# Optimization experiments

Hardware: AMD Instinct MI355X
Metric: run time of the kernel (lower is better)

The kernel has to match this reference:

```python
import jax, jax.numpy as jnp
import numpy as np

N_NODES = 100000
N_EDGES = 3200000
N_GRAPHS = 64


def setup_inputs() -> dict:
    key = jax.random.key(0)
    ks = jax.random.split(key, 9)
    x = jax.random.normal(ks[0], (N_NODES, 3), dtype=jnp.float32)
    edge_index = jax.random.randint(ks[1], (2, N_EDGES), 0, N_NODES, dtype=jnp.int64)
    batch = jnp.sort(jax.random.randint(ks[2], (N_NODES,), 0, N_GRAPHS, dtype=jnp.int64))
    s1 = 1.0 / np.sqrt(3.0)
    s2 = 1.0 / np.sqrt(64.0)
    W1 = jax.random.normal(ks[3], (3, 64), dtype=jnp.float32) * s1
    b1 = jax.random.normal(ks[4], (64,), dtype=jnp.float32) * 0.02
    W2 = jax.random.normal(ks[5], (64, 64), dtype=jnp.float32) * s2
    b2 = jax.random.normal(ks[6], (64,), dtype=jnp.float32) * 0.02
    Wr = jax.random.normal(ks[7], (64, 1), dtype=jnp.float32) * s2
    br = jax.random.normal(ks[8], (1,), dtype=jnp.float32) * 0.02
    return {"x": x, "edge_index": edge_index, "batch": batch,
            "W1": W1, "b1": b1, "W2": W2, "b2": b2, "Wr": Wr, "br": br}


def reference(x, edge_index, batch, W1, b1, W2, b2, Wr, br):
    N = x.shape[0]
    # GCN normalization with self-loops: A_hat = D^-1/2 (A+I) D^-1/2
    loop = jnp.arange(N, dtype=edge_index.dtype)
    src = jnp.concatenate([edge_index[0], loop])  # message sources
    dst = jnp.concatenate([edge_index[1], loop])  # aggregation targets
    deg = jax.ops.segment_sum(jnp.ones(src.shape, jnp.float32), dst, num_segments=N)
    dinv = jnp.where(deg > 0, jax.lax.rsqrt(deg), 0.0)
    norm = dinv[src] * dinv[dst]  # [E+N]

    def conv(h):  # h: [N, F] -> gather, scale, scatter-add
        return jax.ops.segment_sum(norm[:, None] * h[src], dst, num_segments=N)

    h = jax.nn.relu(conv(x @ W1) + b1)
    # dropout(p=0.5) is identity in eval mode
    h = jax.nn.relu(conv(h @ W2) + b2)
    # global mean pool over graphs
    counts = jax.ops.segment_sum(jnp.ones((N,), jnp.float32), batch, num_segments=N_GRAPHS)
    pooled = jax.ops.segment_sum(h, batch, num_segments=N_GRAPHS) / jnp.maximum(counts, 1.0)[:, None]
    return pooled @ Wr + br
```

## Files before the change

kernel.cpp:

```cpp
#include <hip/hip_runtime.h>

#define N_NODES  100000
#define N_EDGES  3200000
#define N_GRAPHS 64
#define NBUCK 391
#define BSH   8
#define TILE  4096
#define CSR_CAP 9216

typedef float v2f __attribute__((ext_vector_type(2)));

__device__ __forceinline__ unsigned pk8(float a, float b, float c, float d) {
    int r = 0;
    r = __builtin_amdgcn_cvt_pk_fp8_f32(a, b, r, false);
    r = __builtin_amdgcn_cvt_pk_fp8_f32(c, d, r, true);
    return (unsigned)r;
}
__device__ __forceinline__ void addfp8(float4& a, unsigned u) {
    v2f lo = __builtin_amdgcn_cvt_pk_f32_fp8((int)u, false);
    v2f hi = __builtin_amdgcn_cvt_pk_f32_fp8((int)u, true);
    a.x += lo[0]; a.y += lo[1]; a.z += hi[0]; a.w += hi[1];
}
__device__ __forceinline__ void fma4(float4& c, float s, const float4& w) {
    c.x += s * w.x; c.y += s * w.y; c.z += s * w.z; c.w += s * w.w;
}

__global__ __launch_bounds__(1024) void k_split(
        const int* __restrict__ src, const int* __restrict__ dst,
        int* __restrict__ gcur, unsigned int* __restrict__ ebuf, int E) {
    __shared__ int hist[512];
    __shared__ int excl_s[512];
    __shared__ int base[NBUCK];
    __shared__ int curs[NBUCK];
    __shared__ int wtot[8];
    __shared__ unsigned int stg[TILE];
    __shared__ unsigned short bkt[TILE];
    int t = threadIdx.x;
    if (t < 512) hist[t] = 0;
    __syncthreads();

    int e0 = blockIdx.x * TILE;
    int nvalid = min(TILE, E - e0);
    int es[4], ed[4];
#pragma unroll
    for (int k = 0; k < 4; ++k) {
        int i = e0 + t + k * 1024;
        if (i < E) {
            es[k] = src[i]; ed[k] = dst[i];
            atomicAdd(&hist[ed[k] >> BSH], 1);
        } else { es[k] = 0; ed[k] = -1; }
    }
    __syncthreads();
    int v = (t < 512) ? hist[t] : 0;
    int lane = t & 63, wvi = t >> 6;
    int val = v;
    for (int off = 1; off < 64; off <<= 1) {
        int u = __shfl_up(val, off);
        if (lane >= off) val += u;
    }
    if (t < 512 && lane == 63) wtot[wvi] = val;
    __syncthreads();
    if (t < 512) {
        int woff = 0;
        for (int w = 0; w < wvi; ++w) woff += wtot[w];
        int texcl = woff + val - v;
        excl_s[t] = texcl;
        if (t < NBUCK) {
            if (v > 0) base[t] = atomicAdd(&gcur[t], v);
            curs[t] = 0;
        }
    }
    __syncthreads();
#pragma unroll
    for (int k = 0; k < 4; ++k) {
        if (ed[k] >= 0) {
            int b = ed[k] >> BSH;
            int r = atomicAdd(&curs[b], 1);
            int pos = excl_s[b] + r;
            stg[pos] = ((unsigned)(ed[k] & 255) << 24) | (unsigned)es[k];
            bkt[pos] = (unsigned short)b;
        }
    }
    __syncthreads();
    for (int j = t; j < nvalid; j += 1024) {
        unsigned p = stg[j];
        int b = bkt[j];
        int pos = base[b] + (j - excl_s[b]);
        if (pos < CSR_CAP) ebuf[(size_t)b * CSR_CAP + pos] = p;
    }
}

__global__ __launch_bounds__(1024) void k_csr(
        const unsigned int* __restrict__ ebuf, const int* __restrict__ gcur,
        int* __restrict__ rowptr, float* __restrict__ dinv, float4* __restrict__ y4,
        const float* __restrict__ x, int* __restrict__ csr_src, int N) {
    __shared__ int ncnt[256];
    __shared__ int nbase[256];
    __shared__ int ncur[256];
    __shared__ int wtot[4];
    __shared__ int sbase;
    __shared__ int stg[CSR_CAP];
    int b = blockIdx.x, t = threadIdx.x;
    int node0 = b << BSH;
    int nodes = min(256, N - node0);
    int cntE = min(gcur[b], CSR_CAP);
    const unsigned int* eb = ebuf + (size_t)b * CSR_CAP;
    if (t < 64) {
        int acc = 0;
        for (int i = t; i < b; i += 64) acc += min(gcur[i], CSR_CAP);
        for (int off = 32; off > 0; off >>= 1) acc += __shfl_down(acc, off);
        if (t == 0) sbase = acc;
    }
    if (t < 256) { ncnt[t] = 0; ncur[t] = 0; }
    __syncthreads();
    int base = sbase;
    if (b == NBUCK - 1 && t == 0) rowptr[N_NODES] = base + cntE;
    for (int j = t; j < cntE; j += 1024) atomicAdd(&ncnt[(int)(eb[j] >> 24)], 1);
    __syncthreads();
    int v = (t < 256) ? ncnt[t] : 0;
    if (t < 256) {
        int lane = t & 63, wv = t >> 6;
        int val = v;
        for (int off = 1; off < 64; off <<= 1) {
            int u = __shfl_up(val, off);
            if (lane >= off) val += u;
        }
        if (lane == 63) wtot[wv] = val;
        __syncthreads();
        int woff = 0;
        for (int w = 0; w < wv; ++w) woff += wtot[w];
        int excl = woff + val - v;
        nbase[t] = excl;
        if (t < nodes) {
            int nn = node0 + t;
            rowptr[nn] = base + excl;
            float dn = rsqrtf((float)(v + 1));
            dinv[nn] = dn;
            y4[nn] = make_float4(dn * x[nn * 3 + 0], dn * x[nn * 3 + 1], dn * x[nn * 3 + 2], 0.f);
        }
    } else {
        __syncthreads();
    }
    __syncthreads();
    for (int j = t; j < cntE; j += 1024) {
        unsigned p = eb[j];
        int ln = (int)(p >> 24);
        int r = atomicAdd(&ncur[ln], 1);
        stg[nbase[ln] + r] = (int)(p & 0xFFFFFFu);
    }
    __syncthreads();
    for (int j = t; j < cntE; j += 1024) csr_src[(size_t)base + j] = stg[j];
}

__global__ __launch_bounds__(256) void k_agg3h1(
        const float4* __restrict__ y4, const int* __restrict__ csr_src,
        const int* __restrict__ rowptr, const float* __restrict__ dinv,
        const float* __restrict__ W1, const float* __restrict__ b1,
        uint4* __restrict__ Hs, int N) {
    int tid = blockIdx.x * blockDim.x + threadIdx.x;
    int n = tid >> 2, q = tid & 3;
    if (n >= N) return;
    int beg = rowptr[n], end = rowptr[n + 1];
    float ax0 = 0.f, ay0 = 0.f, az0 = 0.f;
    float ax1 = 0.f, ay1 = 0.f, az1 = 0.f;
    float ax2 = 0.f, ay2 = 0.f, az2 = 0.f;
    float ax3 = 0.f, ay3 = 0.f, az3 = 0.f;
    if (end > beg) {
        for (int c = beg; c < end; c += 32) {
            int idx[8];
#pragma unroll
            for (int j = 0; j < 8; ++j)
                idx[j] = csr_src[min(c + 4 * j + q, end - 1)];
            float4 v[8];
#pragma unroll
            for (int j = 0; j < 8; ++j) v[j] = y4[idx[j]];
#pragma unroll
            for (int j = 0; j < 8; ++j) {
                bool ok = (c + 4 * j + q) < end;
                float vx = ok ? v[j].x : 0.f;
                float vy = ok ? v[j].y : 0.f;
                float vz = ok ? v[j].z : 0.f;
                if ((j & 3) == 0) { ax0 += vx; ay0 += vy; az0 += vz; }
                if ((j & 3) == 1) { ax1 += vx; ay1 += vy; az1 += vz; }
                if ((j & 3) == 2) { ax2 += vx; ay2 += vy; az2 += vz; }
                if ((j & 3) == 3) { ax3 += vx; ay3 += vy; az3 += vz; }
            }
        }
    }
    float rx = (ax0 + ax1) + (ax2 + ax3);
    float ry = (ay0 + ay1) + (ay2 + ay3);
    float rz = (az0 + az1) + (az2 + az3);
    for (int off = 1; off < 4; off <<= 1) {
        rx += __shfl_xor(rx, off);
        ry += __shfl_xor(ry, off);
        rz += __shfl_xor(rz, off);
    }
    float dn = dinv[n];
    float4 self = y4[n];
    float A0 = dn * (rx + self.x), A1 = dn * (ry + self.y), A2 = dn * (rz + self.z);
    unsigned vals[4];
#pragma unroll
    for (int g = 0; g < 4; ++g) {
        int f = 16 * q + 4 * g;
        float w0 = dn * fmaxf(A0 * W1[f]     + A1 * W1[64 + f]     + A2 * W1[128 + f]     + b1[f],     0.f);
        float w1 = dn * fmaxf(A0 * W1[f + 1] + A1 * W1[64 + f + 1] + A2 * W1[128 + f + 1] + b1[f + 1], 0.f);
        float w2 = dn * fmaxf(A0 * W1[f + 2] + A1 * W1[64 + f + 2] + A2 * W1[128 + f + 2] + b1[f + 2], 0.f);
        float w3 = dn * fmaxf(A0 * W1[f + 3] + A1 * W1[64 + f + 3] + A2 * W1[128 + f + 3] + b1[f + 3], 0.f);
        vals[g] = pk8(w0, w1, w2, w3);
    }
    Hs[(size_t)n * 4 + q] = make_uint4(vals[0], vals[1], vals[2], vals[3]);
}

__global__ __launch_bounds__(256) void k_agg(
        const unsigned int* __restrict__ Hs, const int* __restrict__ csr_src,
        const int* __restrict__ rowptr, const float* __restrict__ dinv,
        float* __restrict__ out, int N) {
    int tid = blockIdx.x * blockDim.x + threadIdx.x;
    int n = tid >> 4, q = tid & 15;
    if (n >= N) return;
    int lane = threadIdx.x & 63;
    int base = lane & ~15;
    int beg = rowptr[n], end = rowptr[n + 1];
    float4 acc0 = make_float4(0.f, 0.f, 0.f, 0.f);
    float4 acc1 = make_float4(0.f, 0.f, 0.f, 0.f);
    float4 acc2 = make_float4(0.f, 0.f, 0.f, 0.f);
    float4 acc3 = make_float4(0.f, 0.f, 0.f, 0.f);
    if (end > beg) {
        int myidx = csr_src[min(beg + q, end - 1)];
        for (int c = beg; c < end; c += 16) {
            int nxt = csr_src[min(c + 16 + q, end - 1)];
            unsigned u[16];
#pragma unroll
            for (int j = 0; j < 16; ++j) {
                int s = __shfl(myidx, base + j);
                u[j] = Hs[(size_t)s * 16 + q];
            }
            int m = end - c;
#pragma unroll
            for (int j = 0; j < 16; ++j) {
                unsigned uj = (j < m) ? u[j] : 0u;
                if ((j & 3) == 0) addfp8(acc0, uj);
                if ((j & 3) == 1) addfp8(acc1, uj);
                if ((j & 3) == 2) addfp8(acc2, uj);
                if ((j & 3) == 3) addfp8(acc3, uj);
            }
            myidx = nxt;
        }
    }
    addfp8(acc0, Hs[(size_t)n * 16 + q]);
    float dn = dinv[n];
    float4 r;
    r.x = dn * ((acc0.x + acc1.x) + (acc2.x + acc3.x));
    r.y = dn * ((acc0.y + acc1.y) + (acc2.y + acc3.y));
    r.z = dn * ((acc0.z + acc1.z) + (acc2.z + acc3.z));
    r.w = dn * ((acc0.w + acc1.w) + (acc2.w + acc3.w));
    ((float4*)(out + (size_t)n * 64))[q] = r;
}

__global__ __launch_bounds__(256) void k_mmpool(
        const float4* __restrict__ A4, const float4* __restrict__ W2v,
        const float* __restrict__ b2, const float* __restrict__ Wr,
        const int* __restrict__ batch, float* __restrict__ gsum,
        float* __restrict__ gcnt, int N) {
    __shared__ float4 W2s[1024];
    __shared__ float lsum[N_GRAPHS];
    __shared__ float lcnt[N_GRAPHS];
    int t = threadIdx.x;
    for (int i = t; i < 1024; i += 256) W2s[i] = W2v[i];
    if (t < N_GRAPHS) { lsum[t] = 0.f; lcnt[t] = 0.f; }
    __syncthreads();

    int f4 = t & 15;
    int ng = t >> 4;
    float4 bb = ((const float4*)b2)[f4];
    float4 wr = ((const float4*)Wr)[f4];
    int base = blockIdx.x * 128;

    for (int tile = 0; tile < 2; ++tile) {
        int n0 = base + tile * 64 + ng * 4;
        int m0 = min(n0 + 0, N - 1), m1 = min(n0 + 1, N - 1);
        int m2 = min(n0 + 2, N - 1), m3 = min(n0 + 3, N - 1);
        const float4* r0 = A4 + (size_t)m0 * 16;
        const float4* r1 = A4 + (size_t)m1 * 16;
        const float4* r2 = A4 + (size_t)m2 * 16;
        const float4* r3 = A4 + (size_t)m3 * 16;
        float4 c0 = make_float4(0.f, 0.f, 0.f, 0.f);
        float4 c1 = make_float4(0.f, 0.f, 0.f, 0.f);
        float4 c2 = make_float4(0.f, 0.f, 0.f, 0.f);
        float4 c3 = make_float4(0.f, 0.f, 0.f, 0.f);
#pragma unroll 4
        for (int ks = 0; ks < 16; ++ks) {
            float4 a0 = r0[ks], a1 = r1[ks], a2 = r2[ks], a3 = r3[ks];
            float4 w0 = W2s[(4 * ks + 0) * 16 + f4];
            float4 w1 = W2s[(4 * ks + 1) * 16 + f4];
            float4 w2 = W2s[(4 * ks + 2) * 16 + f4];
            float4 w3 = W2s[(4 * ks + 3) * 16 + f4];
            fma4(c0, a0.x, w0); fma4(c0, a0.y, w1); fma4(c0, a0.z, w2); fma4(c0, a0.w, w3);
            fma4(c1, a1.x, w0); fma4(c1, a1.y, w1); fma4(c1, a1.z, w2); fma4(c1, a1.w, w3);
            fma4(c2, a2.x, w0); fma4(c2, a2.y, w1); fma4(c2, a2.z, w2); fma4(c2, a2.w, w3);
            fma4(c3, a3.x, w0); fma4(c3, a3.y, w1); fma4(c3, a3.z, w2); fma4(c3, a3.w, w3);
        }
        float p0 = fmaxf(c0.x + bb.x, 0.f) * wr.x + fmaxf(c0.y + bb.y, 0.f) * wr.y +
                   fmaxf(c0.z + bb.z, 0.f) * wr.z + fmaxf(c0.w + bb.w, 0.f) * wr.w;
        float p1 = fmaxf(c1.x + bb.x, 0.f) * wr.x + fmaxf(c1.y + bb.y, 0.f) * wr.y +
                   fmaxf(c1.z + bb.z, 0.f) * wr.z + fmaxf(c1.w + bb.w, 0.f) * wr.w;
        float p2 = fmaxf(c2.x + bb.x, 0.f) * wr.x + fmaxf(c2.y + bb.y, 0.f) * wr.y +
                   fmaxf(c2.z + bb.z, 0.f) * wr.z + fmaxf(c2.w + bb.w, 0.f) * wr.w;
        float p3 = fmaxf(c3.x + bb.x, 0.f) * wr.x + fmaxf(c3.y + bb.y, 0.f) * wr.y +
                   fmaxf(c3.z + bb.z, 0.f) * wr.z + fmaxf(c3.w + bb.w, 0.f) * wr.w;
        for (int off = 8; off > 0; off >>= 1) {
            p0 += __shfl_down(p0, off);
            p1 += __shfl_down(p1, off);
            p2 += __shfl_down(p2, off);
            p3 += __shfl_down(p3, off);
        }
        if (f4 == 0) {
            if (n0 + 0 < N) { int g = batch[n0 + 0]; atomicAdd(&lsum[g], p0); atomicAdd(&lcnt[g], 1.f); }
            if (n0 + 1 < N) { int g = batch[n0 + 1]; atomicAdd(&lsum[g], p1); atomicAdd(&lcnt[g], 1.f); }
            if (n0 + 2 < N) { int g = batch[n0 + 2]; atomicAdd(&lsum[g], p2); atomicAdd(&lcnt[g], 1.f); }
            if (n0 + 3 < N) { int g = batch[n0 + 3]; atomicAdd(&lsum[g], p3); atomicAdd(&lcnt[g], 1.f); }
        }
    }
    __syncthreads();
    if (t < N_GRAPHS && lcnt[t] > 0.0f) {
        atomicAdd(&gsum[t], lsum[t]);
        atomicAdd(&gcnt[t], lcnt[t]);
    }
}

__global__ void k_out(const float* __restrict__ gsum, const float* __restrict__ gcnt,
                      const float* __restrict__ br, float* __restrict__ out) {
    int g = threadIdx.x;
    if (g < N_GRAPHS) out[g] = gsum[g] / fmaxf(gcnt[g], 1.0f) + br[0];
}

extern "C" void kernel_launch(void* const* d_in, const int* in_sizes, int n_in,
                              void* d_out, int out_size, void* d_ws, size_t ws_size,
                              hipStream_t stream) {
    const float* x     = (const float*)d_in[0];
    const int*   ei    = (const int*)d_in[1];
    const int*   batch = (const int*)d_in[2];
    const float* W1    = (const float*)d_in[3];
    const float* b1    = (const float*)d_in[4];
    const float* W2    = (const float*)d_in[5];
    const float* b2    = (const float*)d_in[6];
    const float* Wr    = (const float*)d_in[7];
    const float* br    = (const float*)d_in[8];
    float* out = (float*)d_out;

    const int N = N_NODES, E = N_EDGES;
    const int* src = ei;
    const int* dst = ei + E;

    char* w = (char*)d_ws;
    float* A        = (float*)w; w += (size_t)N * 64 * sizeof(float);
    unsigned int* Hs = (unsigned int*)w; w += (size_t)N * 64;
    int*   csr_src  = (int*)w;   w += (size_t)E * sizeof(int);
    float* dinv     = (float*)w; w += (size_t)N * sizeof(float);
    int*   rowptr   = (int*)w;   w += (size_t)(N + 1) * sizeof(int);
    int*   gcur     = (int*)w;   w += (size_t)NBUCK * sizeof(int);
    float* gsum     = (float*)w; w += N_GRAPHS * sizeof(float);
    float* gcnt     = (float*)w; w += N_GRAPHS * sizeof(float);
    float4* y4      = (float4*)w; w += (size_t)N * sizeof(float4);
    unsigned int* ebuf = (unsigned int*)A;

    hipMemsetAsync(gcur, 0, (size_t)NBUCK * sizeof(int), stream);
    hipMemsetAsync(gsum, 0, N_GRAPHS * sizeof(float), stream);
    hipMemsetAsync(gcnt, 0, N_GRAPHS * sizeof(float), stream);

    k_split<<<(E + TILE - 1) / TILE, 1024, 0, stream>>>(src, dst, gcur, ebuf, E);
    k_csr<<<NBUCK, 1024, 0, stream>>>(ebuf, gcur, rowptr, dinv, y4, x, csr_src, N);

    k_agg3h1<<<(N * 4 + 255) / 256, 256, 0, stream>>>(y4, csr_src, rowptr, dinv,
                                                      W1, b1, (uint4*)Hs, N);

    k_agg<<<(N * 16 + 255) / 256, 256, 0, stream>>>(Hs, csr_src, rowptr, dinv, A, N);
    k_mmpool<<<(N + 127) / 128, 256, 0, stream>>>((const float4*)A, (const float4*)W2,
                                                  b2, Wr, batch, gsum, gcnt, N);

    k_out<<<1, 64, 0, stream>>>(gsum, gcnt, br, out);
}
```

Baseline: 214.0 us.

## Use 16-byte gathers in layer-2 aggregation with cross-lane feature reduction

Each 16-lane node group now splits into 4 edge-parallel subgroups of 4 lanes. Each lane loads a uint4 (16 fp8 features) per neighbor instead of one 4-byte word, so the gather uses fewer, wider memory transactions. Partial sums are combined across subgroups with xor shuffles, and the per-edge broadcast shuffle of source indices is removed. Index loads are nontemporal and prefetched only when another chunk exists. The cost is extra shuffle reduction work and a changed output write pattern.

```diff
diff --git a/kernel.cpp b/kernel.cpp
--- a/kernel.cpp
+++ b/kernel.cpp
@@ -212,49 +212,63 @@
 }
 
 __global__ __launch_bounds__(256) void k_agg(
-        const unsigned int* __restrict__ Hs, const int* __restrict__ csr_src,
+        const uint4* __restrict__ Hs4, const int* __restrict__ csr_src,
         const int* __restrict__ rowptr, const float* __restrict__ dinv,
         float* __restrict__ out, int N) {
     int tid = blockIdx.x * blockDim.x + threadIdx.x;
-    int n = tid >> 4, q = tid & 15;
+    int n = tid >> 4, sub = tid & 15;
     if (n >= N) return;
-    int lane = threadIdx.x & 63;
-    int base = lane & ~15;
+    int p = sub >> 2;
+    int f = sub & 3;
     int beg = rowptr[n], end = rowptr[n + 1];
-    float4 acc0 = make_float4(0.f, 0.f, 0.f, 0.f);
-    float4 acc1 = make_float4(0.f, 0.f, 0.f, 0.f);
-    float4 acc2 = make_float4(0.f, 0.f, 0.f, 0.f);
-    float4 acc3 = make_float4(0.f, 0.f, 0.f, 0.f);
+    float4 a0 = make_float4(0.f, 0.f, 0.f, 0.f);
+    float4 a1 = make_float4(0.f, 0.f, 0.f, 0.f);
+    float4 a2 = make_float4(0.f, 0.f, 0.f, 0.f);
+    float4 a3 = make_float4(0.f, 0.f, 0.f, 0.f);
     if (end > beg) {
-        int myidx = csr_src[min(beg + q, end - 1)];
+        int e[4];
+#pragma unroll
+        for (int j = 0; j < 4; ++j)
+            e[j] = __builtin_nontemporal_load(&csr_src[min(beg + 4 * j + p, end - 1)]);
         for (int c = beg; c < end; c += 16) {
-            int nxt = csr_src[min(c + 16 + q, end - 1)];
-            unsigned u[16];
-#pragma unroll
-            for (int j = 0; j < 16; ++j) {
-                int s = __shfl(myidx, base + j);
-                u[j] = Hs[(size_t)s * 16 + q];
+            uint4 u[4];
+#pragma unroll
+            for (int j = 0; j < 4; ++j)
+                u[j] = Hs4[(size_t)e[j] * 4 + f];
+            int c2 = c + 16;
+            if (c2 < end) {
+#pragma unroll
+                for (int j = 0; j < 4; ++j)
+                    e[j] = __builtin_nontemporal_load(&csr_src[min(c2 + 4 * j + p, end - 1)]);
             }
             int m = end - c;
 #pragma unroll
-            for (int j = 0; j < 16; ++j) {
-                unsigned uj = (j < m) ? u[j] : 0u;
-                if ((j & 3) == 0) addfp8(acc0, uj);
-                if ((j & 3) == 1) addfp8(acc1, uj);
-                if ((j & 3) == 2) addfp8(acc2, uj);
-                if ((j & 3) == 3) addfp8(acc3, uj);
+            for (int j = 0; j < 4; ++j) {
+                uint4 uu = u[j];
+                if (4 * j + p >= m) { uu.x = 0u; uu.y = 0u; uu.z = 0u; uu.w = 0u; }
+                addfp8(a0, uu.x); addfp8(a1, uu.y); addfp8(a2, uu.z); addfp8(a3, uu.w);
             }
-            myidx = nxt;
-        }
-    }
-    addfp8(acc0, Hs[(size_t)n * 16 + q]);
+        }
+    }
+    if (p == 0) {
+        uint4 us = Hs4[(size_t)n * 4 + f];
+        addfp8(a0, us.x); addfp8(a1, us.y); addfp8(a2, us.z); addfp8(a3, us.w);
+    }
+#pragma unroll
+    for (int off = 4; off <= 8; off <<= 1) {
+        a0.x += __shfl_xor(a0.x, off); a0.y += __shfl_xor(a0.y, off);
+        a0.z += __shfl_xor(a0.z, off); a0.w += __shfl_xor(a0.w, off);
+        a1.x += __shfl_xor(a1.x, off); a1.y += __shfl_xor(a1.y, off);
+        a1.z += __shfl_xor(a1.z, off); a1.w += __shfl_xor(a1.w, off);
+        a2.x += __shfl_xor(a2.x, off); a2.y += __shfl_xor(a2.y, off);
+        a2.z += __shfl_xor(a2.z, off); a2.w += __shfl_xor(a2.w, off);
+        a3.x += __shfl_xor(a3.x, off); a3.y += __shfl_xor(a3.y, off);
+        a3.z += __shfl_xor(a3.z, off); a3.w += __shfl_xor(a3.w, off);
+    }
     float dn = dinv[n];
-    float4 r;
-    r.x = dn * ((acc0.x + acc1.x) + (acc2.x + acc3.x));
-    r.y = dn * ((acc0.y + acc1.y) + (acc2.y + acc3.y));
-    r.z = dn * ((acc0.z + acc1.z) + (acc2.z + acc3.z));
-    r.w = dn * ((acc0.w + acc1.w) + (acc2.w + acc3.w));
-    ((float4*)(out + (size_t)n * 64))[q] = r;
+    float4 w = (p == 0) ? a0 : (p == 1) ? a1 : (p == 2) ? a2 : a3;
+    w.x *= dn; w.y *= dn; w.z *= dn; w.w *= dn;
+    ((float4*)(out + (size_t)n * 64))[f * 4 + p] = w;
 }
 
 __global__ __launch_bounds__(256) void k_mmpool(
@@ -374,7 +388,8 @@
     k_agg3h1<<<(N * 4 + 255) / 256, 256, 0, stream>>>(y4, csr_src, rowptr, dinv,
                                                       W1, b1, (uint4*)Hs, N);
 
-    k_agg<<<(N * 16 + 255) / 256, 256, 0, stream>>>(Hs, csr_src, rowptr, dinv, A, N);
+    k_agg<<<(N * 16 + 255) / 256, 256, 0, stream>>>((const uint4*)Hs, csr_src, rowptr,
+                                                    dinv, A, N);
     k_mmpool<<<(N + 127) / 128, 256, 0, stream>>>((const float4*)A, (const float4*)W2,
                                                   b2, Wr, batch, gsum, gcnt, N);
 
```

Result: no change. 216.9 us (+1.3%).

## Fuse second-layer aggregation with W2 matmul, ReLU, readout and pooling

Applied to the files above, without the earlier changes.

Merges the fp8 gather-aggregate kernel with the dense W2 matmul and mean-pool kernel. Each 16-lane group now holds an aggregated node row in registers, broadcasts it with shuffles and multiplies against W2 staged in shared memory. This removes writing and re-reading the N x 64 fp32 intermediate and one kernel launch. In exchange every block loads W2 into LDS, uses 512-thread blocks, and drops the n<N guard because N*16 divides evenly by 512.

```diff
diff --git a/kernel.cpp b/kernel.cpp
--- a/kernel.cpp
+++ b/kernel.cpp
@@ -211,14 +211,23 @@
     Hs[(size_t)n * 4 + q] = make_uint4(vals[0], vals[1], vals[2], vals[3]);
 }
 
-__global__ __launch_bounds__(256) void k_agg(
+__global__ __launch_bounds__(512) void k_aggmm(
         const unsigned int* __restrict__ Hs, const int* __restrict__ csr_src,
         const int* __restrict__ rowptr, const float* __restrict__ dinv,
-        float* __restrict__ out, int N) {
-    int tid = blockIdx.x * blockDim.x + threadIdx.x;
+        const float4* __restrict__ W2v, const float* __restrict__ b2,
+        const float* __restrict__ Wr, const int* __restrict__ batch,
+        float* __restrict__ gsum, float* __restrict__ gcnt, int N) {
+    __shared__ float4 W2s[1024];
+    __shared__ float lsum[N_GRAPHS];
+    __shared__ float lcnt[N_GRAPHS];
+    int t = threadIdx.x;
+    for (int i = t; i < 1024; i += 512) W2s[i] = W2v[i];
+    if (t < N_GRAPHS) { lsum[t] = 0.f; lcnt[t] = 0.f; }
+    __syncthreads();
+
+    int tid = blockIdx.x * 512 + t;
     int n = tid >> 4, q = tid & 15;
-    if (n >= N) return;
-    int lane = threadIdx.x & 63;
+    int lane = t & 63;
     int base = lane & ~15;
     int beg = rowptr[n], end = rowptr[n + 1];
     float4 acc0 = make_float4(0.f, 0.f, 0.f, 0.f);
@@ -254,72 +263,31 @@
     r.y = dn * ((acc0.y + acc1.y) + (acc2.y + acc3.y));
     r.z = dn * ((acc0.z + acc1.z) + (acc2.z + acc3.z));
     r.w = dn * ((acc0.w + acc1.w) + (acc2.w + acc3.w));
-    ((float4*)(out + (size_t)n * 64))[q] = r;
-}
-
-__global__ __launch_bounds__(256) void k_mmpool(
-        const float4* __restrict__ A4, const float4* __restrict__ W2v,
-        const float* __restrict__ b2, const float* __restrict__ Wr,
-        const int* __restrict__ batch, float* __restrict__ gsum,
-        float* __restrict__ gcnt, int N) {
-    __shared__ float4 W2s[1024];
-    __shared__ float lsum[N_GRAPHS];
-    __shared__ float lcnt[N_GRAPHS];
-    int t = threadIdx.x;
-    for (int i = t; i < 1024; i += 256) W2s[i] = W2v[i];
-    if (t < N_GRAPHS) { lsum[t] = 0.f; lcnt[t] = 0.f; }
-    __syncthreads();
-
-    int f4 = t & 15;
-    int ng = t >> 4;
-    float4 bb = ((const float4*)b2)[f4];
-    float4 wr = ((const float4*)Wr)[f4];
-    int base = blockIdx.x * 128;
-
-    for (int tile = 0; tile < 2; ++tile) {
-        int n0 = base + tile * 64 + ng * 4;
-        int m0 = min(n0 + 0, N - 1), m1 = min(n0 + 1, N - 1);
-        int m2 = min(n0 + 2, N - 1), m3 = min(n0 + 3, N - 1);
-        const float4* r0 = A4 + (size_t)m0 * 16;
-        const float4* r1 = A4 + (size_t)m1 * 16;
-        const float4* r2 = A4 + (size_t)m2 * 16;
-        const float4* r3 = A4 + (size_t)m3 * 16;
-        float4 c0 = make_float4(0.f, 0.f, 0.f, 0.f);
-        float4 c1 = make_float4(0.f, 0.f, 0.f, 0.f);
-        float4 c2 = make_float4(0.f, 0.f, 0.f, 0.f);
-        float4 c3 = make_float4(0.f, 0.f, 0.f, 0.f);
+
+    float4 bb = ((const float4*)b2)[q];
+    float4 wr = ((const float4*)Wr)[q];
+    float4 cacc = make_float4(0.f, 0.f, 0.f, 0.f);
 #pragma unroll 4
-        for (int ks = 0; ks < 16; ++ks) {
-            float4 a0 = r0[ks], a1 = r1[ks], a2 = r2[ks], a3 = r3[ks];
-            float4 w0 = W2s[(4 * ks + 0) * 16 + f4];
-            float4 w1 = W2s[(4 * ks + 1) * 16 + f4];
-            float4 w2 = W2s[(4 * ks + 2) * 16 + f4];
-            float4 w3 = W2s[(4 * ks + 3) * 16 + f4];
-            fma4(c0, a0.x, w0); fma4(c0, a0.y, w1); fma4(c0, a0.z, w2); fma4(c0, a0.w, w3);
-            fma4(c1, a1.x, w0); fma4(c1, a1.y, w1); fma4(c1, a1.z, w2); fma4(c1, a1.w, w3);
-            fma4(c2, a2.x, w0); fma4(c2, a2.y, w1); fma4(c2, a2.z, w2); fma4(c2, a2.w, w3);
-            fma4(c3, a3.x, w0); fma4(c3, a3.y, w1); fma4(c3, a3.z, w2); fma4(c3, a3.w, w3);
-        }
-        float p0 = fmaxf(c0.x + bb.x, 0.f) * wr.x + fmaxf(c0.y + bb.y, 0.f) * wr.y +
-                   fmaxf(c0.z + bb.z, 0.f) * wr.z + fmaxf(c0.w + bb.w, 0.f) * wr.w;
-        float p1 = fmaxf(c1.x + bb.x, 0.f) * wr.x + fmaxf(c1.y + bb.y, 0.f) * wr.y +
-                   fmaxf(c1.z + bb.z, 0.f) * wr.z + fmaxf(c1.w + bb.w, 0.f) * wr.w;
-        float p2 = fmaxf(c2.x + bb.x, 0.f) * wr.x + fmaxf(c2.y + bb.y, 0.f) * wr.y +
-                   fmaxf(c2.z + bb.z, 0.f) * wr.z + fmaxf(c2.w + bb.w, 0.f) * wr.w;
-        float p3 = fmaxf(c3.x + bb.x, 0.f) * wr.x + fmaxf(c3.y + bb.y, 0.f) * wr.y +
-                   fmaxf(c3.z + bb.z, 0.f) * wr.z + fmaxf(c3.w + bb.w, 0.f) * wr.w;
-        for (int off = 8; off > 0; off >>= 1) {
-            p0 += __shfl_down(p0, off);
-            p1 += __shfl_down(p1, off);
-            p2 += __shfl_down(p2, off);
-            p3 += __shfl_down(p3, off);
-        }
-        if (f4 == 0) {
-            if (n0 + 0 < N) { int g = batch[n0 + 0]; atomicAdd(&lsum[g], p0); atomicAdd(&lcnt[g], 1.f); }
-            if (n0 + 1 < N) { int g = batch[n0 + 1]; atomicAdd(&lsum[g], p1); atomicAdd(&lcnt[g], 1.f); }
-            if (n0 + 2 < N) { int g = batch[n0 + 2]; atomicAdd(&lsum[g], p2); atomicAdd(&lcnt[g], 1.f); }
-            if (n0 + 3 < N) { int g = batch[n0 + 3]; atomicAdd(&lsum[g], p3); atomicAdd(&lcnt[g], 1.f); }
-        }
+    for (int ks = 0; ks < 16; ++ks) {
+        float ax = __shfl(r.x, base + ks);
+        float ay = __shfl(r.y, base + ks);
+        float az = __shfl(r.z, base + ks);
+        float aw = __shfl(r.w, base + ks);
+        fma4(cacc, ax, W2s[(4 * ks + 0) * 16 + q]);
+        fma4(cacc, ay, W2s[(4 * ks + 1) * 16 + q]);
+        fma4(cacc, az, W2s[(4 * ks + 2) * 16 + q]);
+        fma4(cacc, aw, W2s[(4 * ks + 3) * 16 + q]);
+    }
+    float p = fmaxf(cacc.x + bb.x, 0.f) * wr.x + fmaxf(cacc.y + bb.y, 0.f) * wr.y +
+              fmaxf(cacc.z + bb.z, 0.f) * wr.z + fmaxf(cacc.w + bb.w, 0.f) * wr.w;
+    p += __shfl_xor(p, 1);
+    p += __shfl_xor(p, 2);
+    p += __shfl_xor(p, 4);
+    p += __shfl_xor(p, 8);
+    if (q == 0) {
+        int g = batch[n];
+        atomicAdd(&lsum[g], p);
+        atomicAdd(&lcnt[g], 1.f);
     }
     __syncthreads();
     if (t < N_GRAPHS && lcnt[t] > 0.0f) {
@@ -374,9 +342,9 @@
     k_agg3h1<<<(N * 4 + 255) / 256, 256, 0, stream>>>(y4, csr_src, rowptr, dinv,
                                                       W1, b1, (uint4*)Hs, N);
 
-    k_agg<<<(N * 16 + 255) / 256, 256, 0, stream>>>(Hs, csr_src, rowptr, dinv, A, N);
-    k_mmpool<<<(N + 127) / 128, 256, 0, stream>>>((const float4*)A, (const float4*)W2,
-                                                  b2, Wr, batch, gsum, gcnt, N);
+    k_aggmm<<<(N * 16) / 512, 512, 0, stream>>>(Hs, csr_src, rowptr, dinv,
+                                                (const float4*)W2, b2, Wr, batch,
+                                                gsum, gcnt, N);
 
     k_out<<<1, 64, 0, stream>>>(gsum, gcnt, br, out);
 }
```

Result: no change. 214.3 us (+0.2%).
